# Kernel optimization log

Measured on AMD Instinct MI355X. Metric: run time of the kernel, lower is better.

The kernel has to match this reference:

```python
import jax, jax.numpy as jnp
import numpy as np

KERNEL = 128
STRIDE = 64


def setup_inputs() -> dict:
    key = jax.random.key(0)
    k1, k2, k3 = jax.random.split(key, 3)
    in_features = 8192
    fold_num = (in_features - KERNEL) // STRIDE + 1  # 127
    local_features = 128
    batch = 2048
    x = jax.random.normal(k1, (batch, in_features), dtype=jnp.float32)
    # stacked per-window Linear weights/biases (PyTorch Linear: y = x @ W.T + b)
    bound = 1.0 / np.sqrt(KERNEL)
    W = jax.random.uniform(k2, (fold_num, local_features, KERNEL), dtype=jnp.float32,
                           minval=-bound, maxval=bound)
    b = jax.random.uniform(k3, (fold_num, local_features), dtype=jnp.float32,
                           minval=-bound, maxval=bound)
    return {"x": x, "W": W, "b": b}


def reference(x, W, b):
    fold_num = W.shape[0]
    # window gather indices: [fold_num, kernel]
    idx = STRIDE * jnp.arange(fold_num)[:, None] + jnp.arange(KERNEL)[None, :]
    windows = x[:, idx]                      # [batch, fold_num, kernel]
    # per-window linear: out[b,f,l] = sum_k windows[b,f,k] * W[f,l,k] + b[f,l]
    out = jnp.einsum('bfk,flk->bfl', windows, W) + b[None, :, :]
    # concat along feature dim as in torch.cat(..., 1)
    return out.reshape(out.shape[0], -1)     # [batch, fold_num*local_features]
```

## Files before the change

kernel.cpp:

```cpp
#include <hip/hip_runtime.h>
#include <hip/hip_bf16.h>

typedef float f32x4 __attribute__((ext_vector_type(4)));
typedef __bf16 bf16x8 __attribute__((ext_vector_type(8)));

#define INF   8192
#define FOLDS 127
#define LOCAL 128
#define OUTF  (FOLDS * LOCAL)
#define BM    128
#define MT_PER_BLOCK 4

__device__ __forceinline__ void cvt_store8(char* lds, int byte, f32x4 v0, f32x4 v1) {
    bf16x8 w;
    w[0] = (__bf16)v0[0]; w[1] = (__bf16)v0[1]; w[2] = (__bf16)v0[2]; w[3] = (__bf16)v0[3];
    w[4] = (__bf16)v1[0]; w[5] = (__bf16)v1[1]; w[6] = (__bf16)v1[2]; w[7] = (__bf16)v1[3];
    *(bf16x8*)(lds + byte) = w;
}

__global__ __launch_bounds__(256, 2)
void local_linear_kernel(const float* __restrict__ x,
                         const float* __restrict__ W,
                         const float* __restrict__ bias,
                         float* __restrict__ out)
{
    __shared__ __align__(16) __bf16 As[128 * 128];
    __shared__ __align__(16) __bf16 Bs[128 * 128];

    const int f = blockIdx.x;
    const int c = blockIdx.y;
    const int t = threadIdx.x;

    const int lane = t & 63;
    const int wid  = t >> 6;
    const int wm   = wid >> 1;
    const int wn   = wid & 1;
    const int r16  = lane & 15;
    const int kq   = lane >> 4;

    const float* __restrict__ Wf = W + (size_t)f * (LOCAL * 128);
    #pragma unroll
    for (int it = 0; it < 8; ++it) {
        const int e   = it * 2048 + t * 8;
        const int row = e >> 7;
        const int col = e & 127;
        const float* g = Wf + row * 128 + col;
        f32x4 v0 = *(const f32x4*)g;
        f32x4 v1 = *(const f32x4*)(g + 4);
        cvt_store8((char*)Bs, (row * 256 + col * 2) ^ ((row & 7) << 4), v0, v1);
    }

    float bv[4];
    #pragma unroll
    for (int j = 0; j < 4; ++j)
        bv[j] = bias[f * LOCAL + wn * 64 + j * 16 + r16];

    for (int im = 0; im < MT_PER_BLOCK; ++im) {
        const int mt = c * MT_PER_BLOCK + im;
        const int m0 = mt * BM;
        const float* __restrict__ xg = x + (size_t)m0 * INF + (size_t)f * 64;

        #pragma unroll
        for (int it = 0; it < 8; ++it) {
            const int e   = it * 2048 + t * 8;
            const int row = e >> 7;
            const int col = e & 127;
            const float* g = xg + (size_t)row * INF + col;
            f32x4 v0 = *(const f32x4*)g;
            f32x4 v1 = *(const f32x4*)(g + 4);
            cvt_store8((char*)As, (row * 256 + col * 2) ^ ((row & 7) << 4), v0, v1);
        }
        __syncthreads();

        f32x4 acc[4][4];
        #pragma unroll
        for (int i = 0; i < 4; ++i)
            #pragma unroll
            for (int j = 0; j < 4; ++j)
                acc[i][j] = (f32x4){bv[j], bv[j], bv[j], bv[j]};

        #pragma unroll
        for (int ks = 0; ks < 4; ++ks) {
            const int kof = ks * 32 + kq * 8;
            bf16x8 a[4], b[4];
            #pragma unroll
            for (int i = 0; i < 4; ++i) {
                const int row  = wm * 64 + i * 16 + r16;
                const int byte = (row * 256 + kof * 2) ^ ((row & 7) << 4);
                a[i] = *(const bf16x8*)((const char*)As + byte);
            }
            #pragma unroll
            for (int j = 0; j < 4; ++j) {
                const int row  = wn * 64 + j * 16 + r16;
                const int byte = (row * 256 + kof * 2) ^ ((row & 7) << 4);
                b[j] = *(const bf16x8*)((const char*)Bs + byte);
            }
            #pragma unroll
            for (int i = 0; i < 4; ++i)
                #pragma unroll
                for (int j = 0; j < 4; ++j)
                    acc[i][j] = __builtin_amdgcn_mfma_f32_16x16x32_bf16(a[i], b[j], acc[i][j], 0, 0, 0);
        }

        #pragma unroll
        for (int i = 0; i < 4; ++i) {
            const int mrow = m0 + wm * 64 + i * 16 + kq * 4;
            #pragma unroll
            for (int j = 0; j < 4; ++j) {
                const int ncol = f * LOCAL + wn * 64 + j * 16 + r16;
                float* o = out + (size_t)mrow * OUTF + ncol;
                #pragma unroll
                for (int r = 0; r < 4; ++r)
                    o[(size_t)r * OUTF] = acc[i][j][r];
            }
        }
        __syncthreads();
    }
}

extern "C" void kernel_launch(void* const* d_in, const int* in_sizes, int n_in,
                              void* d_out, int out_size, void* d_ws, size_t ws_size,
                              hipStream_t stream) {
    const float* x    = (const float*)d_in[0];
    const float* W    = (const float*)d_in[1];
    const float* bias = (const float*)d_in[2];
    float* out        = (float*)d_out;

    dim3 grid(FOLDS, 2048 / (BM * MT_PER_BLOCK));
    dim3 block(256);
    local_linear_kernel<<<grid, block, 0, stream>>>(x, W, bias, out);
}
```

Before: 55.08 us.

## Drop LDS staging and load MFMA operands directly from global memory

```diff
diff --git a/kernel.cpp b/kernel.cpp
--- a/kernel.cpp
+++ b/kernel.cpp
@@ -9,28 +9,27 @@
 #define LOCAL 128
 #define OUTF  (FOLDS * LOCAL)
 #define BM    128
-#define MT_PER_BLOCK 4
 
-__device__ __forceinline__ void cvt_store8(char* lds, int byte, f32x4 v0, f32x4 v1) {
+__device__ __forceinline__ bf16x8 load_cvt8(const float* __restrict__ g) {
+    f32x4 v0 = *(const f32x4*)g;
+    f32x4 v1 = *(const f32x4*)(g + 4);
     bf16x8 w;
     w[0] = (__bf16)v0[0]; w[1] = (__bf16)v0[1]; w[2] = (__bf16)v0[2]; w[3] = (__bf16)v0[3];
     w[4] = (__bf16)v1[0]; w[5] = (__bf16)v1[1]; w[6] = (__bf16)v1[2]; w[7] = (__bf16)v1[3];
-    *(bf16x8*)(lds + byte) = w;
+    return w;
 }
 
-__global__ __launch_bounds__(256, 2)
+__global__ __launch_bounds__(256, 3)
 void local_linear_kernel(const float* __restrict__ x,
                          const float* __restrict__ W,
                          const float* __restrict__ bias,
                          float* __restrict__ out)
 {
-    __shared__ __align__(16) __bf16 As[128 * 128];
-    __shared__ __align__(16) __bf16 Bs[128 * 128];
+    const int f  = blockIdx.x;
+    const int mt = blockIdx.y;
+    const int t  = threadIdx.x;
 
-    const int f = blockIdx.x;
-    const int c = blockIdx.y;
-    const int t = threadIdx.x;
-
+    const int m0   = mt * BM;
     const int lane = t & 63;
     const int wid  = t >> 6;
     const int wm   = wid >> 1;
@@ -38,83 +37,49 @@
     const int r16  = lane & 15;
     const int kq   = lane >> 4;
 
-    const float* __restrict__ Wf = W + (size_t)f * (LOCAL * 128);
-    #pragma unroll
-    for (int it = 0; it < 8; ++it) {
-        const int e   = it * 2048 + t * 8;
-        const int row = e >> 7;
-        const int col = e & 127;
-        const float* g = Wf + row * 128 + col;
-        f32x4 v0 = *(const f32x4*)g;
-        f32x4 v1 = *(const f32x4*)(g + 4);
-        cvt_store8((char*)Bs, (row * 256 + col * 2) ^ ((row & 7) << 4), v0, v1);
-    }
+    const float* __restrict__ xw = x + (size_t)(m0 + wm * 64) * INF + (size_t)f * 64;
+    const float* __restrict__ Ww = W + (size_t)f * (LOCAL * 128) + (size_t)(wn * 64) * 128;
 
     float bv[4];
     #pragma unroll
     for (int j = 0; j < 4; ++j)
         bv[j] = bias[f * LOCAL + wn * 64 + j * 16 + r16];
 
-    for (int im = 0; im < MT_PER_BLOCK; ++im) {
-        const int mt = c * MT_PER_BLOCK + im;
-        const int m0 = mt * BM;
-        const float* __restrict__ xg = x + (size_t)m0 * INF + (size_t)f * 64;
+    f32x4 acc[4][4];
+    #pragma unroll
+    for (int i = 0; i < 4; ++i)
+        #pragma unroll
+        for (int j = 0; j < 4; ++j)
+            acc[i][j] = (f32x4){bv[j], bv[j], bv[j], bv[j]};
 
+    #pragma unroll
+    for (int ks = 0; ks < 4; ++ks) {
+        const int kof = ks * 32 + kq * 8;
+        bf16x8 a[4], b[4];
         #pragma unroll
-        for (int it = 0; it < 8; ++it) {
-            const int e   = it * 2048 + t * 8;
-            const int row = e >> 7;
-            const int col = e & 127;
-            const float* g = xg + (size_t)row * INF + col;
-            f32x4 v0 = *(const f32x4*)g;
-            f32x4 v1 = *(const f32x4*)(g + 4);
-            cvt_store8((char*)As, (row * 256 + col * 2) ^ ((row & 7) << 4), v0, v1);
-        }
-        __syncthreads();
-
-        f32x4 acc[4][4];
+        for (int i = 0; i < 4; ++i)
+            a[i] = load_cvt8(xw + (size_t)(i * 16 + r16) * INF + kof);
+        #pragma unroll
+        for (int j = 0; j < 4; ++j)
+            b[j] = load_cvt8(Ww + (j * 16 + r16) * 128 + kof);
         #pragma unroll
         for (int i = 0; i < 4; ++i)
             #pragma unroll
             for (int j = 0; j < 4; ++j)
-                acc[i][j] = (f32x4){bv[j], bv[j], bv[j], bv[j]};
+                acc[i][j] = __builtin_amdgcn_mfma_f32_16x16x32_bf16(a[i], b[j], acc[i][j], 0, 0, 0);
+    }
 
+    #pragma unroll
+    for (int i = 0; i < 4; ++i) {
+        const int mrow = m0 + wm * 64 + i * 16 + kq * 4;
         #pragma unroll
-        for (int ks = 0; ks < 4; ++ks) {
-            const int kof = ks * 32 + kq * 8;
-            bf16x8 a[4], b[4];
+        for (int j = 0; j < 4; ++j) {
+            const int ncol = f * LOCAL + wn * 64 + j * 16 + r16;
+            float* o = out + (size_t)mrow * OUTF + ncol;
             #pragma unroll
-            for (int i = 0; i < 4; ++i) {
-                const int row  = wm * 64 + i * 16 + r16;
-                const int byte = (row * 256 + kof * 2) ^ ((row & 7) << 4);
-                a[i] = *(const bf16x8*)((const char*)As + byte);
-            }
-            #pragma unroll
-            for (int j = 0; j < 4; ++j) {
-                const int row  = wn * 64 + j * 16 + r16;
-                const int byte = (row * 256 + kof * 2) ^ ((row & 7) << 4);
-                b[j] = *(const bf16x8*)((const char*)Bs + byte);
-            }
-            #pragma unroll
-            for (int i = 0; i < 4; ++i)
-                #pragma unroll
-                for (int j = 0; j < 4; ++j)
-                    acc[i][j] = __builtin_amdgcn_mfma_f32_16x16x32_bf16(a[i], b[j], acc[i][j], 0, 0, 0);
+            for (int r = 0; r < 4; ++r)
+                o[(size_t)r * OUTF] = acc[i][j][r];
         }
-
-        #pragma unroll
-        for (int i = 0; i < 4; ++i) {
-            const int mrow = m0 + wm * 64 + i * 16 + kq * 4;
-            #pragma unroll
-            for (int j = 0; j < 4; ++j) {
-                const int ncol = f * LOCAL + wn * 64 + j * 16 + r16;
-                float* o = out + (size_t)mrow * OUTF + ncol;
-                #pragma unroll
-                for (int r = 0; r < 4; ++r)
-                    o[(size_t)r * OUTF] = acc[i][j][r];
-            }
-        }
-        __syncthreads();
     }
 }
 
@@ -126,7 +91,7 @@
     const float* bias = (const float*)d_in[2];
     float* out        = (float*)d_out;
 
-    dim3 grid(FOLDS, 2048 / (BM * MT_PER_BLOCK));
+    dim3 grid(FOLDS, 2048 / BM);
     dim3 block(256);
     local_linear_kernel<<<grid, block, 0, stream>>>(x, W, bias, out);
 }
```

Result: slower. 88.27 us (+60.3%).
